# Kernel tuning notes

Measured on AMD Instinct MI355X. Metric: run time of the kernel, lower is better.

Reference implementation:

```python
import jax, jax.numpy as jnp
import numpy as np

T, B, E, L, V = 128, 256, 1024, 1024, 95


def setup_inputs() -> dict:
    key = jax.random.key(0)
    ks = jax.random.split(key, 10)
    x = jax.random.randint(ks[0], (T, B), 0, V, dtype=jnp.int64)  # [T, B] time-major tokens
    h = jnp.zeros((B, L), dtype=jnp.float32)                       # initial hidden state
    emb = jax.random.normal(ks[1], (V, E), dtype=jnp.float32) * 0.02
    s = 1.0 / np.sqrt(E + L)
    Wf = jax.random.uniform(ks[2], (L, E + L), jnp.float32, -s, s)
    bf = jax.random.uniform(ks[3], (L,), jnp.float32, -s, s)
    Wi = jax.random.uniform(ks[4], (L, E + L), jnp.float32, -s, s)
    bi = jax.random.uniform(ks[5], (L,), jnp.float32, -s, s)
    Wo = jax.random.uniform(ks[6], (L, E + L), jnp.float32, -s, s)
    bo = jax.random.uniform(ks[7], (L,), jnp.float32, -s, s)
    Wc = jax.random.uniform(ks[8], (L, E + L), jnp.float32, -s, s)
    bc = jax.random.uniform(ks[9], (L,), jnp.float32, -s, s)
    return {"x": x, "h": h, "emb": emb, "Wf": Wf, "bf": bf, "Wi": Wi,
            "bi": bi, "Wo": Wo, "bo": bo, "Wc": Wc, "bc": bc}


def reference(x, h, emb, Wf, bf, Wi, bi, Wo, bo, Wc, bc):
    # Fuse the 4 gate linears into one [E+L, 4L] GEMM per step (same math).
    W_all = jnp.concatenate([Wf, Wi, Wo, Wc], axis=0).T  # [E+L, 4L]
    b_all = jnp.concatenate([bf, bi, bo, bc], axis=0)     # [4L]
    embedded = emb[x]                                      # [T, B, E]
    c0 = jnp.zeros_like(h)

    def step(carry, e_t):
        h, c = carry
        entry = jnp.concatenate([e_t, h], axis=1)          # [B, E+L]
        g = entry @ W_all + b_all                          # [B, 4L]
        f, i, o, cg = jnp.split(g, 4, axis=1)
        c = jax.nn.sigmoid(f) * c + jax.nn.sigmoid(i) * jnp.tanh(cg)
        h = jax.nn.sigmoid(o) * jnp.tanh(c)
        return (h, c), h

    _, hs = jax.lax.scan(step, (h, c0), embedded)
    return hs  # [T, B, L]
```

## Files before the change

### kernel.cpp

```cpp
#include <hip/hip_runtime.h>
#include <stdint.h>

constexpr int TT = 128;
constexpr int BB = 256;
constexpr int LL = 1024;
constexpr int NG = 4096;
constexpr int VV = 95;

typedef short bf16x8 __attribute__((ext_vector_type(8)));
typedef float f32x4  __attribute__((ext_vector_type(4)));

typedef __attribute__((address_space(1))) const uint32_t gu32;
typedef __attribute__((address_space(3))) uint32_t lu32;

__device__ __forceinline__ unsigned short f2bf(float f) {
    unsigned int u = __builtin_bit_cast(unsigned int, f);
    unsigned int r = (u + 0x7FFFu + ((u >> 16) & 1u)) >> 16;
    return (unsigned short)r;
}
__device__ __forceinline__ float bf2f(unsigned short h) {
    unsigned int u = ((unsigned int)h) << 16;
    return __builtin_bit_cast(float, u);
}
__device__ __forceinline__ float sigmoidf_(float x) {
    return 1.0f / (1.0f + __expf(-x));
}
__device__ __forceinline__ float tanhf_(float x) {
    return 1.0f - 2.0f / (__expf(2.0f * x) + 1.0f);
}

__global__ void prep_w_all(const float* __restrict__ Wf, const float* __restrict__ Wi,
                           const float* __restrict__ Wo, const float* __restrict__ Wc,
                           unsigned short* __restrict__ Wimg,
                           unsigned short* __restrict__ Wemb_hi,
                           unsigned short* __restrict__ Wemb_lo) {
    int idx = blockIdx.x * 256 + threadIdx.x;
    const int total = NG * 2048;
    for (; idx < total; idx += gridDim.x * 256) {
        int row = idx >> 11;
        int col = idx & 2047;
        int lt   = row >> 6;
        int nl   = row & 63;
        int gate = nl >> 4;
        int l    = lt * 16 + (nl & 15);
        const float* W = (gate == 0) ? Wf : (gate == 1) ? Wi : (gate == 2) ? Wo : Wc;
        float w = W[l * 2048 + col];
        if (col >= 1024) {
            int k = col - 1024;
            size_t byte = (size_t)lt * 131072 + (size_t)(k >> 5) * 4096 + nl * 64 + (k & 31) * 2;
            *(unsigned short*)((char*)Wimg + byte) = f2bf(w);
        } else {
            unsigned short hi = f2bf(w);
            float lo = w - bf2f(hi);
            Wemb_hi[row * 1024 + col] = hi;
            Wemb_lo[row * 1024 + col] = f2bf(lo);
        }
    }
}

__global__ void prep_emb_split(const float* __restrict__ emb,
                               unsigned short* __restrict__ Eh,
                               unsigned short* __restrict__ El) {
    int idx = blockIdx.x * 256 + threadIdx.x;
    int v = idx >> 10;
    float w = (v < VV) ? emb[idx] : 0.0f;
    unsigned short hi = f2bf(w);
    Eh[idx] = hi;
    El[idx] = f2bf(w - bf2f(hi));
}

__global__ __launch_bounds__(128)
void gate_pre_mfma(const unsigned short* __restrict__ Eh, const unsigned short* __restrict__ El,
                   const unsigned short* __restrict__ Wh, const unsigned short* __restrict__ Wl,
                   const float* __restrict__ bfv, const float* __restrict__ biv,
                   const float* __restrict__ bov, const float* __restrict__ bcv,
                   float* __restrict__ gp2) {
    const int lt   = blockIdx.x;
    const int tid  = threadIdx.x;
    const int lane = tid & 63;
    const int wm   = tid >> 6;
    const int l15  = lane & 15;
    const int kq   = lane >> 4;

    f32x4 acc[3][4];
    #pragma unroll
    for (int mf = 0; mf < 3; ++mf)
        #pragma unroll
        for (int nf = 0; nf < 4; ++nf) acc[mf][nf] = (f32x4){0.f, 0.f, 0.f, 0.f};

    #pragma unroll 2
    for (int ks = 0; ks < 32; ++ks) {
        const int k0 = ks * 32 + kq * 8;
        bf16x8 ah[3], al[3], bh[4], bl[4];
        #pragma unroll
        for (int mf = 0; mf < 3; ++mf) {
            const size_t ao = (size_t)(wm * 48 + mf * 16 + l15) * 1024 + k0;
            ah[mf] = *(const bf16x8*)(Eh + ao);
            al[mf] = *(const bf16x8*)(El + ao);
        }
        #pragma unroll
        for (int nf = 0; nf < 4; ++nf) {
            const size_t bo = (size_t)(lt * 64 + nf * 16 + l15) * 1024 + k0;
            bh[nf] = *(const bf16x8*)(Wh + bo);
            bl[nf] = *(const bf16x8*)(Wl + bo);
        }
        #pragma unroll
        for (int mf = 0; mf < 3; ++mf)
            #pragma unroll
            for (int nf = 0; nf < 4; ++nf) {
                acc[mf][nf] = __builtin_amdgcn_mfma_f32_16x16x32_bf16(ah[mf], bh[nf], acc[mf][nf], 0, 0, 0);
                acc[mf][nf] = __builtin_amdgcn_mfma_f32_16x16x32_bf16(ah[mf], bl[nf], acc[mf][nf], 0, 0, 0);
                acc[mf][nf] = __builtin_amdgcn_mfma_f32_16x16x32_bf16(al[mf], bh[nf], acc[mf][nf], 0, 0, 0);
            }
    }

    const int lgl = lt * 16 + l15;
    #pragma unroll
    for (int nf = 0; nf < 4; ++nf) {
        const float* bias = (nf == 0) ? bfv : (nf == 1) ? biv : (nf == 2) ? bov : bcv;
        const float bv = bias[lgl];
        #pragma unroll
        for (int mf = 0; mf < 3; ++mf)
            #pragma unroll
            for (int r = 0; r < 4; ++r) {
                const int v = wm * 48 + mf * 16 + kq * 4 + r;
                if (v < VV)
                    gp2[((size_t)v * LL + lgl) * 4 + nf] = acc[mf][nf][r] + bv;
            }
    }
}

__global__ void init_state(const float* __restrict__ h_init,
                           unsigned short* __restrict__ h0,
                           unsigned int* __restrict__ flags) {
    int idx = blockIdx.x * 256 + threadIdx.x;
    h0[idx] = f2bf(h_init[idx]);
    if (idx < 4096) flags[idx] = 0;
}

__global__ __launch_bounds__(256, 1)
void lstm_all(const unsigned short* __restrict__ Wimg,
              const float* __restrict__ gp2,
              const int* __restrict__ x,
              unsigned short* __restrict__ hb0,
              unsigned short* __restrict__ hb1,
              float* __restrict__ out,
              unsigned int* __restrict__ flags) {
    __shared__ unsigned short wlds_s[65536];
    char* wlds = (char*)wlds_s;

    const int tid  = threadIdx.x;
    const int lane = tid & 63;
    const int wv   = tid >> 6;
    const int bt   = blockIdx.x >> 6;
    const int lt   = blockIdx.x & 63;
    const int l15  = lane & 15;
    const int kq   = lane >> 4;

    const int l  = lt * 16 + l15;
    const int b0 = bt * 64 + wv * 16 + kq * 4;

    {
        const char* wsrc = (const char*)Wimg + (size_t)lt * 131072 + tid * 16;
        #pragma unroll
        for (int j = 0; j < 32; ++j)
            __builtin_amdgcn_global_load_lds((gu32*)(wsrc + j * 4096),
                                             (lu32*)(wlds + j * 4096 + wv * 1024),
                                             16, 0, 0);
        asm volatile("s_waitcnt vmcnt(0)" ::: "memory");
        __syncthreads();
    }
    const char* bbase = wlds + l15 * 64 + kq * 16;

    const size_t arow = (size_t)(bt * 64 + wv * 16 + l15) * 2048 + kq * 16;
    const char* aptr0 = (const char*)hb0 + arow;
    const char* aptr1 = (const char*)hb1 + arow;
    const unsigned int* fp[4];
    #pragma unroll
    for (int q = 0; q < 4; ++q) fp[q] = flags + (((bt << 6) + (q << 4) + l15) << 4);
    const int myflag = ((bt << 6) + lt) << 4;

    float c_r[4] = {0.f, 0.f, 0.f, 0.f};
    float* out_t = out;

    #define SB __builtin_amdgcn_sched_barrier(0);

    #define POLL(q)                                                              \
        { unsigned int fv;                                                       \
          for (;;) {                                                             \
            asm volatile("global_load_dword %0, %1, off sc0 sc1\n\t"             \
                         "s_waitcnt vmcnt(0)"                                    \
                         : "=v"(fv) : "v"(fp[q]) : "memory");                    \
            if (__all((int)(fv >= (unsigned int)t))) break;                      \
            __builtin_amdgcn_s_sleep(1);                                         \
          } }

    #define ISSUEA(buf, q)                                                       \
        _Pragma("unroll") for (int ki = 0; ki < 8; ++ki) {                       \
            const char* ap = aptr + ((q) * 8 + ki) * 64;                         \
            asm volatile("global_load_dwordx4 %0, %1, off sc0 sc1"               \
                         : "=v"(buf[ki]) : "v"(ap));                             \
        }

    #define QCOMP(areg, q)                                                       \
        _Pragma("unroll") for (int ki = 0; ki < 8; ++ki) {                       \
            const int ks = (q) * 8 + ki;                                         \
            const char* bc = bbase + ks * 4096;                                  \
            bf16x8 bw0 = *(const bf16x8*)(bc);                                   \
            bf16x8 bw1 = *(const bf16x8*)(bc + 1024);                            \
            bf16x8 bw2 = *(const bf16x8*)(bc + 2048);                            \
            bf16x8 bw3 = *(const bf16x8*)(bc + 3072);                            \
            acc[0] = __builtin_amdgcn_mfma_f32_16x16x32_bf16(areg[ki], bw0, acc[0], 0, 0, 0); \
            acc[1] = __builtin_amdgcn_mfma_f32_16x16x32_bf16(areg[ki], bw1, acc[1], 0, 0, 0); \
            acc[2] = __builtin_amdgcn_mfma_f32_16x16x32_bf16(areg[ki], bw2, acc[2], 0, 0, 0); \
            acc[3] = __builtin_amdgcn_mfma_f32_16x16x32_bf16(areg[ki], bw3, acc[3], 0, 0, 0); \
        }

    for (int t = 0; t < TT; ++t) {
        const char* aptr = (t & 1) ? aptr1 : aptr0;
        unsigned short* hout = (t & 1) ? hb0 : hb1;
        const int* xt = x + t * BB;

        f32x4 acc[4];
        #pragma unroll
        for (int nf = 0; nf < 4; ++nf) acc[nf] = (f32x4){0.f, 0.f, 0.f, 0.f};
        bf16x8 bufA[8], bufB[8];

        int4 xv;
        asm volatile("global_load_dwordx4 %0, %1, off sc0 sc1"
                     : "=v"(xv) : "v"(xt + b0));

        POLL(0)
        ISSUEA(bufA, 0)
        POLL(1)
        ISSUEA(bufB, 1)
        SB QCOMP(bufA, 0) SB
        POLL(2)
        ISSUEA(bufA, 2)
        SB QCOMP(bufB, 1) SB
        POLL(3)
        ISSUEA(bufB, 3)
        float4 gpv[4];
        {
            const int vr[4] = {xv.x, xv.y, xv.z, xv.w};
            #pragma unroll
            for (int r = 0; r < 4; ++r) {
                const float* gpp = gp2 + ((size_t)vr[r] * LL + l) * 4;
                asm volatile("global_load_dwordx4 %0, %1, off"
                             : "=v"(gpv[r]) : "v"(gpp));
            }
        }
        SB QCOMP(bufA, 2) SB
        asm volatile("s_waitcnt vmcnt(0)" ::: "memory");
        SB
        QCOMP(bufB, 3)

        #pragma unroll
        for (int r = 0; r < 4; ++r) {
            const float gf = acc[0][r] + gpv[r].x;
            const float gi = acc[1][r] + gpv[r].y;
            const float go = acc[2][r] + gpv[r].z;
            const float gc = acc[3][r] + gpv[r].w;
            const float cn = sigmoidf_(gf) * c_r[r] + sigmoidf_(gi) * tanhf_(gc);
            const float hn = sigmoidf_(go) * tanhf_(cn);
            c_r[r] = cn;
            const size_t off = (size_t)(b0 + r) * LL + l;
            out_t[off] = hn;
            unsigned int hbits = f2bf(hn);
            const unsigned short* hp = hout + off;
            asm volatile("global_store_short %0, %1, off sc0 sc1"
                         :: "v"(hp), "v"(hbits) : "memory");
        }

        asm volatile("s_waitcnt vmcnt(0)" ::: "memory");
        __syncthreads();
        if (t < TT - 1 && tid == 0)
            atomicExch(&flags[myflag], (unsigned int)(t + 1));
        out_t += BB * LL;
    }

    #undef SB
    #undef POLL
    #undef ISSUEA
    #undef QCOMP
}

extern "C" void kernel_launch(void* const* d_in, const int* in_sizes, int n_in,
                              void* d_out, int out_size, void* d_ws, size_t ws_size,
                              hipStream_t stream) {
    const int*   x      = (const int*)d_in[0];
    const float* h_init = (const float*)d_in[1];
    const float* emb    = (const float*)d_in[2];
    const float* Wf     = (const float*)d_in[3];
    const float* bfv    = (const float*)d_in[4];
    const float* Wi     = (const float*)d_in[5];
    const float* biv    = (const float*)d_in[6];
    const float* Wo     = (const float*)d_in[7];
    const float* bov    = (const float*)d_in[8];
    const float* Wc     = (const float*)d_in[9];
    const float* bcv    = (const float*)d_in[10];
    float* out = (float*)d_out;

    char* ws = (char*)d_ws;
    unsigned short* Wimg    = (unsigned short*)(ws);
    unsigned short* Wemb_hi = (unsigned short*)(ws + 8388608);
    unsigned short* Wemb_lo = (unsigned short*)(ws + 16777216);
    unsigned short* Eh      = (unsigned short*)(ws + 25165824);
    unsigned short* El      = (unsigned short*)(ws + 25362432);
    float*          gp2     = (float*)(ws + 25559040);
    unsigned short* hb0     = (unsigned short*)(ws + 27131904);
    unsigned short* hb1     = (unsigned short*)(ws + 27656192);
    unsigned int*   flags   = (unsigned int*)(ws + 28180480);

    prep_w_all<<<4096, 256, 0, stream>>>(Wf, Wi, Wo, Wc, Wimg, Wemb_hi, Wemb_lo);
    prep_emb_split<<<384, 256, 0, stream>>>(emb, Eh, El);
    gate_pre_mfma<<<64, 128, 0, stream>>>(Eh, El, Wemb_hi, Wemb_lo,
                                          bfv, biv, bov, bcv, gp2);
    init_state<<<1024, 256, 0, stream>>>(h_init, hb0, flags);

    void* kargs[] = {(void*)&Wimg, (void*)&gp2, (void*)&x,
                     (void*)&hb0, (void*)&hb1, (void*)&out, (void*)&flags};
    hipLaunchCooperativeKernel(reinterpret_cast<void*>(lstm_all),
                               dim3(256), dim3(256), kargs, 0, stream);
}
```

Before: 1.038 ms.

## Swizzle LDS weight layout, poll all flags once, and pipeline loads with vmcnt

The weight image is now written with an XOR swizzle of the 16-byte k-slices by row, and the LDS B reads use the matching swizzle, to reduce bank conflicts. Instead of four staged flag polls interleaved with the hidden-state loads, each wave polls all 64 producer flags once up front. Loads are then double-buffered with explicit partial vmcnt waits. The h bf16 stores are issued before the fp32 output stores, so the barrier waits only on the h stores. This trades the earlier overlap of polling with compute for a single sync point plus tighter load pipelining.

New measurement: 965.2 us. 1.08x faster.

```diff
diff --git a/kernel.cpp b/kernel.cpp
--- a/kernel.cpp
+++ b/kernel.cpp
@@ -47,7 +47,9 @@
         float w = W[l * 2048 + col];
         if (col >= 1024) {
             int k = col - 1024;
-            size_t byte = (size_t)lt * 131072 + (size_t)(k >> 5) * 4096 + nl * 64 + (k & 31) * 2;
+            int ksl = ((k >> 3) & 3) ^ (nl & 3);
+            size_t byte = (size_t)lt * 131072 + (size_t)(k >> 5) * 4096 + nl * 64
+                        + (ksl << 4) + (k & 7) * 2;
             *(unsigned short*)((char*)Wimg + byte) = f2bf(w);
         } else {
             unsigned short hi = f2bf(w);
@@ -139,13 +141,13 @@
 }
 
 __global__ __launch_bounds__(256, 1)
-void lstm_all(const unsigned short* __restrict__ Wimg,
-              const float* __restrict__ gp2,
-              const int* __restrict__ x,
-              unsigned short* __restrict__ hb0,
-              unsigned short* __restrict__ hb1,
-              float* __restrict__ out,
-              unsigned int* __restrict__ flags) {
+void lstm_all3(const unsigned short* __restrict__ Wimg,
+               const float* __restrict__ gp2,
+               const int* __restrict__ x,
+               unsigned short* __restrict__ hb0,
+               unsigned short* __restrict__ hb1,
+               float* __restrict__ out,
+               unsigned int* __restrict__ flags) {
     __shared__ unsigned short wlds_s[65536];
     char* wlds = (char*)wlds_s;
 
@@ -170,14 +172,12 @@
         asm volatile("s_waitcnt vmcnt(0)" ::: "memory");
         __syncthreads();
     }
-    const char* bbase = wlds + l15 * 64 + kq * 16;
+    const char* bbase = wlds + l15 * 64 + ((kq ^ (l15 & 3)) << 4);
 
     const size_t arow = (size_t)(bt * 64 + wv * 16 + l15) * 2048 + kq * 16;
     const char* aptr0 = (const char*)hb0 + arow;
     const char* aptr1 = (const char*)hb1 + arow;
-    const unsigned int* fp[4];
-    #pragma unroll
-    for (int q = 0; q < 4; ++q) fp[q] = flags + (((bt << 6) + (q << 4) + l15) << 4);
+    const unsigned int* fpoll = flags + (((bt << 6) + lane) << 4);
     const int myflag = ((bt << 6) + lt) << 4;
 
     float c_r[4] = {0.f, 0.f, 0.f, 0.f};
@@ -185,12 +185,12 @@
 
     #define SB __builtin_amdgcn_sched_barrier(0);
 
-    #define POLL(q)                                                              \
+    #define POLLALL()                                                            \
         { unsigned int fv;                                                       \
           for (;;) {                                                             \
             asm volatile("global_load_dword %0, %1, off sc0 sc1\n\t"             \
                          "s_waitcnt vmcnt(0)"                                    \
-                         : "=v"(fv) : "v"(fp[q]) : "memory");                    \
+                         : "=&v"(fv) : "v"(fpoll) : "memory");                   \
             if (__all((int)(fv >= (unsigned int)t))) break;                      \
             __builtin_amdgcn_s_sleep(1);                                         \
           } }
@@ -199,7 +199,7 @@
         _Pragma("unroll") for (int ki = 0; ki < 8; ++ki) {                       \
             const char* ap = aptr + ((q) * 8 + ki) * 64;                         \
             asm volatile("global_load_dwordx4 %0, %1, off sc0 sc1"               \
-                         : "=v"(buf[ki]) : "v"(ap));                             \
+                         : "=&v"(buf[ki]) : "v"(ap));                            \
         }
 
     #define QCOMP(areg, q)                                                       \
@@ -216,6 +216,8 @@
             acc[3] = __builtin_amdgcn_mfma_f32_16x16x32_bf16(areg[ki], bw3, acc[3], 0, 0, 0); \
         }
 
+    #define WAITV(N) asm volatile("s_waitcnt vmcnt(" #N ")" ::: "memory");
+
     for (int t = 0; t < TT; ++t) {
         const char* aptr = (t & 1) ? aptr1 : aptr0;
         unsigned short* hout = (t & 1) ? hb0 : hb1;
@@ -226,20 +228,20 @@
         for (int nf = 0; nf < 4; ++nf) acc[nf] = (f32x4){0.f, 0.f, 0.f, 0.f};
         bf16x8 bufA[8], bufB[8];
 
+        POLLALL()
+        SB
+
         int4 xv;
-        asm volatile("global_load_dwordx4 %0, %1, off sc0 sc1"
-                     : "=v"(xv) : "v"(xt + b0));
-
-        POLL(0)
+        {
+            const int* xp = xt + b0;
+            asm volatile("global_load_dwordx4 %0, %1, off"
+                         : "=&v"(xv) : "v"(xp));
+        }
         ISSUEA(bufA, 0)
-        POLL(1)
         ISSUEA(bufB, 1)
-        SB QCOMP(bufA, 0) SB
-        POLL(2)
-        ISSUEA(bufA, 2)
-        SB QCOMP(bufB, 1) SB
-        POLL(3)
-        ISSUEA(bufB, 3)
+        SB
+        WAITV(8)
+        SB
         float4 gpv[4];
         {
             const int vr[4] = {xv.x, xv.y, xv.z, xv.w};
@@ -247,14 +249,24 @@
             for (int r = 0; r < 4; ++r) {
                 const float* gpp = gp2 + ((size_t)vr[r] * LL + l) * 4;
                 asm volatile("global_load_dwordx4 %0, %1, off"
-                             : "=v"(gpv[r]) : "v"(gpp));
+                             : "=&v"(gpv[r]) : "v"(gpp));
             }
         }
-        SB QCOMP(bufA, 2) SB
-        asm volatile("s_waitcnt vmcnt(0)" ::: "memory");
+        SB
+        QCOMP(bufA, 0) SB
+        ISSUEA(bufA, 2) SB
+        WAITV(12)
+        SB
+        QCOMP(bufB, 1) SB
+        ISSUEA(bufB, 3) SB
+        WAITV(8)
+        SB
+        QCOMP(bufA, 2) SB
+        WAITV(0)
         SB
         QCOMP(bufB, 3)
 
+        float hnew[4];
         #pragma unroll
         for (int r = 0; r < 4; ++r) {
             const float gf = acc[0][r] + gpv[r].x;
@@ -262,17 +274,22 @@
             const float go = acc[2][r] + gpv[r].z;
             const float gc = acc[3][r] + gpv[r].w;
             const float cn = sigmoidf_(gf) * c_r[r] + sigmoidf_(gi) * tanhf_(gc);
-            const float hn = sigmoidf_(go) * tanhf_(cn);
+            hnew[r] = sigmoidf_(go) * tanhf_(cn);
             c_r[r] = cn;
+        }
+        #pragma unroll
+        for (int r = 0; r < 4; ++r) {
             const size_t off = (size_t)(b0 + r) * LL + l;
-            out_t[off] = hn;
-            unsigned int hbits = f2bf(hn);
+            unsigned int hbits = f2bf(hnew[r]);
             const unsigned short* hp = hout + off;
             asm volatile("global_store_short %0, %1, off sc0 sc1"
                          :: "v"(hp), "v"(hbits) : "memory");
         }
-
-        asm volatile("s_waitcnt vmcnt(0)" ::: "memory");
+        #pragma unroll
+        for (int r = 0; r < 4; ++r)
+            out_t[(size_t)(b0 + r) * LL + l] = hnew[r];
+
+        WAITV(4)
         __syncthreads();
         if (t < TT - 1 && tid == 0)
             atomicExch(&flags[myflag], (unsigned int)(t + 1));
@@ -280,9 +297,10 @@
     }
 
     #undef SB
-    #undef POLL
+    #undef POLLALL
     #undef ISSUEA
     #undef QCOMP
+    #undef WAITV
 }
 
 extern "C" void kernel_launch(void* const* d_in, const int* in_sizes, int n_in,
@@ -320,6 +338,6 @@
 
     void* kargs[] = {(void*)&Wimg, (void*)&gp2, (void*)&x,
                      (void*)&hb0, (void*)&hb1, (void*)&out, (void*)&flags};
-    hipLaunchCooperativeKernel(reinterpret_cast<void*>(lstm_all),
+    hipLaunchCooperativeKernel(reinterpret_cast<void*>(lstm_all3),
                                dim3(256), dim3(256), kargs, 0, stream);
 }
```
